# Kernel optimization log

Measured on AMD Instinct MI355X. Metric: run time of the kernel, lower is better.

Reference implementation:

```python
import jax, jax.numpy as jnp
import numpy as np

T, D, H, E, K = 4096, 1024, 2048, 8, 2  # tokens, model dim, expert hidden, n_experts, top_k
AUX_COEF = 0.01


def setup_inputs() -> dict:
    key = jax.random.key(0)
    ks = jax.random.split(key, 8)
    sd = lambda fan_in: 1.0 / np.sqrt(fan_in)
    x = jax.random.normal(ks[0], (T, D), jnp.float32)
    Wr = jax.random.normal(ks[1], (E, D), jnp.float32) * sd(D)      # router (no bias)
    w1 = jax.random.normal(ks[2], (E, H, D), jnp.float32) * sd(D)   # stacked up-proj
    w2 = jax.random.normal(ks[3], (E, D, H), jnp.float32) * sd(H)   # stacked down-proj
    w3 = jax.random.normal(ks[4], (E, H, D), jnp.float32) * sd(D)   # stacked gate-proj
    w1s = jax.random.normal(ks[5], (H, D), jnp.float32) * sd(D)     # shared expert
    w2s = jax.random.normal(ks[6], (D, H), jnp.float32) * sd(H)
    w3s = jax.random.normal(ks[7], (H, D), jnp.float32) * sd(D)
    return dict(x=x, Wr=Wr, w1=w1, w2=w2, w3=w3, w1s=w1s, w2s=w2s, w3s=w3s)


def _gelu(v):
    return jax.nn.gelu(v, approximate=False)  # torch F.gelu default = exact erf


def reference(x, Wr, w1, w2, w3, w1s, w2s, w3s):
    n_tok = x.shape[0]
    router_out = x @ Wr.T                                   # [T, E]
    router_probs = jax.nn.softmax(router_out, axis=-1)
    _, topk_idx = jax.lax.top_k(router_out, K)              # [T, K]
    topk_probs, _ = jax.lax.top_k(router_probs, K)          # top-k of probs (same order)

    # auxiliary load-balance loss (first-choice density * mean prob)
    expert_mask = jax.nn.one_hot(topk_idx[:, 0], E, dtype=jnp.float32)
    density = expert_mask.mean(axis=0)
    aux_loss = AUX_COEF * jnp.sum(density * router_probs.mean(axis=0)) * E

    # combine weights C[t, e] = sum of routed probs for expert e at token t
    C = jnp.zeros((n_tok, E), x.dtype).at[
        jnp.arange(n_tok)[:, None], topk_idx
    ].add(topk_probs)

    # dense per-expert SwiGLU-style FFN, combined by C (equal math to
    # sort-based dispatch + scatter_add in the original)
    h = _gelu(jnp.einsum('td,ehd->teh', x, w1)) * jnp.einsum('td,ehd->teh', x, w3)
    ye = jnp.einsum('teh,edh->ted', h, w2)                  # [T, E, D]
    out = jnp.einsum('ted,te->td', ye, C)

    # shared expert (always active)
    out = out + (_gelu(x @ w1s.T) * (x @ w3s.T)) @ w2s.T
    return out, aux_loss
```

## Files before the change

kernel.cpp:

```cpp
#include <hip/hip_runtime.h>
#include <hip/hip_bf16.h>
#include <cstdint>

#define T_TOK 4096
#define DMODEL 1024
#define HDIM 2048

typedef short bf16x8 __attribute__((ext_vector_type(8)));
typedef float f32x4 __attribute__((ext_vector_type(4)));
typedef uint32_t u32x4 __attribute__((ext_vector_type(4)));

__device__ __forceinline__ uint32_t cvt_pk_bf16(float lo, float hi) {
  uint32_t d;
  asm("v_cvt_pk_bf16_f32 %0, %1, %2" : "=v"(d) : "v"(lo), "v"(hi));
  return d;
}
__device__ __forceinline__ unsigned short f2bf(float f) {
  uint32_t d;
  asm("v_cvt_pk_bf16_f32 %0, %1, %1" : "=v"(d) : "v"(f));
  return (unsigned short)d;
}
__device__ __forceinline__ float gelu_fast(float v) {
  float z = v * 0.70710678118654752f;
  float az = fabsf(z);
  float t = __frcp_rn(1.0f + 0.3275911f * az);
  float poly = ((((1.061405429f * t - 1.453152027f) * t + 1.421413741f) * t
                 - 0.284496736f) * t + 0.254829592f) * t;
  float er = 1.0f - poly * __expf(-z * z);
  er = (z < 0.f) ? -er : er;
  return 0.5f * v * (1.0f + er);
}
__device__ __forceinline__ void gload16(const void* g, void* lds) {
  __builtin_amdgcn_global_load_lds((const __attribute__((address_space(1))) void*)g,
                                   (__attribute__((address_space(3))) void*)lds, 16, 0, 0);
}
__device__ __forceinline__ u32x4 pk8(const float* s) {
  float4 v0 = ((const float4*)s)[0], v1 = ((const float4*)s)[1];
  u32x4 p = {cvt_pk_bf16(v0.x, v0.y), cvt_pk_bf16(v0.z, v0.w),
             cvt_pk_bf16(v1.x, v1.y), cvt_pk_bf16(v1.z, v1.w)};
  return p;
}
__device__ __forceinline__ int xcd_remap(int d, int nblk) {
  int q = nblk >> 3, r = nblk & 7, xc = d & 7, i = d >> 3;
  return (xc < r ? xc * (q + 1) : r * (q + 1) + (xc - r) * q) + i;
}

__global__ __launch_bounds__(256) void convert_w(
    const float* __restrict__ w1, const float* __restrict__ w3,
    const float* __restrict__ w1s, const float* __restrict__ w3s,
    const float* __restrict__ w2, const float* __restrict__ w2s,
    short* __restrict__ wB, short* __restrict__ wd) {
  int bid = blockIdx.x;
  if (bid < 18432) {
    int id = bid * 256 + threadIdx.x;
    int e = id >> 19, rem = id & 524287;
    int nf = rem >> 11, k32 = (rem >> 6) & 31, ln = rem & 63;
    int h = (nf >> 1) * 16 + (ln & 15);
    size_t so = (size_t)h * DMODEL + k32 * 32 + (ln >> 4) * 8;
    const float* src = (nf & 1)
        ? ((e < 8) ? w3 + (size_t)e * 2097152 + so : w3s + so)
        : ((e < 8) ? w1 + (size_t)e * 2097152 + so : w1s + so);
    *(u32x4*)(wB + (size_t)id * 8) = pk8(src);
  } else {
    int id = (bid - 18432) * 256 + threadIdx.x;
    int e = id >> 18, rem = id & 262143;
    int d16 = rem >> 12, h32 = (rem >> 6) & 63, ln = rem & 63;
    size_t so = (size_t)(d16 * 16 + (ln & 15)) * HDIM + h32 * 32 + (ln >> 4) * 8;
    const float* s2 = (e < 8) ? w2 + (size_t)e * 2097152 + so : w2s + so;
    *(u32x4*)(wd + (size_t)id * 8) = pk8(s2);
  }
}

__global__ __launch_bounds__(256) void router_kernel(
    const float* __restrict__ x, const float* __restrict__ Wr,
    int* __restrict__ cursor, int* __restrict__ cnt1,
    float* __restrict__ psum, int* __restrict__ perm,
    int* __restrict__ tokpos, float* __restrict__ wtok,
    short* __restrict__ xb) {
  __shared__ float4 sW[8 * 256];
  __shared__ float sP[8];
  int tid = threadIdx.x;
  const float4* W4 = (const float4*)Wr;
  for (int i = tid; i < 2048; i += 256) sW[i] = W4[i];
  if (tid < 8) sP[tid] = 0.f;
  __syncthreads();

  int lane = tid & 63, wid = tid >> 6;
  int t = blockIdx.x * 4 + wid;
  float acc[8] = {0.f, 0.f, 0.f, 0.f, 0.f, 0.f, 0.f, 0.f};
  const float4* x4 = (const float4*)(x + (size_t)t * DMODEL);
#pragma unroll
  for (int it = 0; it < 4; ++it) {
    float4 xv = x4[it * 64 + lane];
    uint2 pk = {cvt_pk_bf16(xv.x, xv.y), cvt_pk_bf16(xv.z, xv.w)};
    *(uint2*)(xb + (size_t)t * DMODEL + it * 256 + lane * 4) = pk;
#pragma unroll
    for (int e = 0; e < 8; ++e) {
      float4 wv = sW[e * 256 + it * 64 + lane];
      acc[e] += xv.x * wv.x + xv.y * wv.y + xv.z * wv.z + xv.w * wv.w;
    }
  }
#pragma unroll
  for (int e = 0; e < 8; ++e)
    for (int off = 32; off; off >>= 1) acc[e] += __shfl_xor(acc[e], off);

  float mx = acc[0];
#pragma unroll
  for (int e = 1; e < 8; ++e) mx = fmaxf(mx, acc[e]);
  float ex[8], s = 0.f;
#pragma unroll
  for (int e = 0; e < 8; ++e) { ex[e] = expf(acc[e] - mx); s += ex[e]; }
  float inv = 1.f / s;
  int e0 = 0;
#pragma unroll
  for (int e = 1; e < 8; ++e) if (acc[e] > acc[e0]) e0 = e;
  int e1 = (e0 == 0) ? 1 : 0;
#pragma unroll
  for (int e = 0; e < 8; ++e) if (e != e0 && acc[e] > acc[e1]) e1 = e;

  if (lane == 0) {
#pragma unroll
    for (int e = 0; e < 8; ++e) atomicAdd(&sP[e], ex[e] * inv);
    atomicAdd(&cnt1[e0], 1);
    int s0 = atomicAdd(&cursor[e0], 1);
    perm[e0 * 4096 + s0] = t;
    int s1 = atomicAdd(&cursor[e1], 1);
    perm[e1 * 4096 + s1] = t;
    tokpos[2 * t] = (e0 << 12) | s0;
    tokpos[2 * t + 1] = (e1 << 12) | s1;
    wtok[2 * t] = ex[e0] * inv;
    wtok[2 * t + 1] = ex[e1] * inv;
  }
  __syncthreads();
  if (tid < 8) atomicAdd(&psum[tid], sP[tid]);
}

__global__ void finalize_kernel(const int* __restrict__ cursor,
                                const int* __restrict__ cnt1,
                                const float* __restrict__ psum,
                                int* __restrict__ base,
                                int* __restrict__ work, int* __restrict__ nwork,
                                float* __restrict__ aux_out) {
  if (threadIdx.x == 0) {
    int b = 0, a = 0;
    for (int e = 0; e < 9; ++e) {
      int c = (e < 8) ? cursor[e] : 4096;
      base[e] = b;
      int t1 = (c + 127) >> 7;
      for (int mt = 0; mt < t1; ++mt) work[a++] = (e << 8) | mt;
      b += t1 << 7;
    }
    *nwork = a;
    float aux = 0.f;
    for (int e = 0; e < 8; ++e)
      aux += ((float)cnt1[e] * (1.f / T_TOK)) * (psum[e] * (1.f / T_TOK));
    aux_out[0] = 0.01f * 8.f * aux;
  }
}

__global__ __launch_bounds__(256, 3) void gemm_upgate(
    const short* __restrict__ xb, const short* __restrict__ wB,
    const int* __restrict__ cursor, const int* __restrict__ base,
    const int* __restrict__ work, const int* __restrict__ nwork,
    const int* __restrict__ perm, unsigned short* __restrict__ hbuf) {
  int nblk = *nwork * 32;
  int d = blockIdx.x;
  if (d >= nblk) return;
  int o = xcd_remap(d, nblk);
  int y = o >> 5, nt = o & 31;
  int wk = work[y];
  int e = wk >> 8, mt = wk & 255;
  int cnt = (e < 8) ? cursor[e] : 4096;
  int hb = base[e];
  const short* wE = wB + (size_t)e * 4194304;

  __shared__ short lds[16384];

  int tid = threadIdx.x, lane = tid & 63, wid = tid >> 6;
  int fr = lane & 15, q4r = lane >> 4;
  int wm = wid >> 1, wn = wid & 1;

  size_t aOff[2], bOff[2];
#pragma unroll
  for (int c = 0; c < 2; ++c) {
    int g = c * 4 + wid;
    int slot = mt * 128 + g * 16 + fr;
    int tok = (e == 8) ? slot : ((slot < cnt) ? perm[e * 4096 + slot] : 0);
    aOff[c] = (size_t)tok * DMODEL + q4r * 8;
    bOff[c] = (size_t)(nt * 8 + g) * 32 * 512 + lane * 8;
  }

  auto stage = [&](int b, int t) {
#pragma unroll
    for (int c = 0; c < 2; ++c) {
      int g = c * 4 + wid;
      gload16(xb + aOff[c] + t * 32, &lds[b * 8192 + g * 512 + lane * 8]);
      gload16(wE + bOff[c] + (size_t)t * 512,
              &lds[b * 8192 + 4096 + g * 512 + lane * 8]);
    }
  };

  f32x4 acc[4][4] = {};

  auto compute = [&](int b) {
    bf16x8 af[4], bf[4];
#pragma unroll
    for (int m = 0; m < 4; ++m)
      af[m] = *(const bf16x8*)&lds[b * 8192 + (wm * 4 + m) * 512 + lane * 8];
#pragma unroll
    for (int n = 0; n < 4; ++n)
      bf[n] = *(const bf16x8*)&lds[b * 8192 + 4096 + (wn * 4 + n) * 512 + lane * 8];
    __builtin_amdgcn_s_setprio(1);
#pragma unroll
    for (int m = 0; m < 4; ++m)
#pragma unroll
      for (int n = 0; n < 4; ++n)
        acc[m][n] = __builtin_amdgcn_mfma_f32_16x16x32_bf16(af[m], bf[n], acc[m][n], 0, 0, 0);
    __builtin_amdgcn_s_setprio(0);
  };

  stage(0, 0);
  __syncthreads();
  int b = 0;
#pragma unroll 1
  for (int t = 0; t < 32; ++t) {
    if (t < 31) stage(b ^ 1, t + 1);
    compute(b);
    __syncthreads();
    b ^= 1;
  }

#pragma unroll
  for (int m = 0; m < 4; ++m) {
#pragma unroll
    for (int p = 0; p < 2; ++p) {
      f32x4 u = acc[m][2 * p], g = acc[m][2 * p + 1];
      int hcol = (nt * 4 + wn * 2 + p) * 16 + fr;
#pragma unroll
      for (int j = 0; j < 4; ++j) {
        int sl = mt * 128 + wm * 64 + m * 16 + q4r * 4 + j;
        float hv = (sl < cnt) ? gelu_fast(u[j]) * g[j] : 0.f;
        hbuf[(size_t)(hb + sl) * HDIM + hcol] = f2bf(hv);
      }
    }
  }
}

__global__ __launch_bounds__(256, 3) void gemm_down(
    const unsigned short* __restrict__ hbuf, const short* __restrict__ wd,
    const int* __restrict__ base,
    const int* __restrict__ work, const int* __restrict__ nwork,
    float* __restrict__ ybuf) {
  int nblk = *nwork * 8;
  int d = blockIdx.x;
  if (d >= nblk) return;
  int o = xcd_remap(d, nblk);
  int y = o >> 3, nt = o & 7;
  int wk = work[y];
  int e = wk >> 8, mt = wk & 255;
  int hb = base[e];
  const short* wdE = wd + (size_t)e * 2097152;

  __shared__ short lds[16384];

  int tid = threadIdx.x, lane = tid & 63, wid = tid >> 6;
  int fr = lane & 15, q4r = lane >> 4;
  int wm = wid >> 1, wn = wid & 1;

  size_t aOff[2], bOff[2];
#pragma unroll
  for (int c = 0; c < 2; ++c) {
    int g = c * 4 + wid;
    aOff[c] = (size_t)(hb + mt * 128 + g * 16 + fr) * HDIM + q4r * 8;
    bOff[c] = (size_t)(nt * 8 + g) * 64 * 512 + lane * 8;
  }

  auto stage = [&](int b, int t) {
#pragma unroll
    for (int c = 0; c < 2; ++c) {
      int g = c * 4 + wid;
      gload16(hbuf + aOff[c] + t * 32, &lds[b * 8192 + g * 512 + lane * 8]);
      gload16(wdE + bOff[c] + (size_t)t * 512,
              &lds[b * 8192 + 4096 + g * 512 + lane * 8]);
    }
  };

  f32x4 acc[4][4] = {};

  auto compute = [&](int b) {
    bf16x8 af[4], bf[4];
#pragma unroll
    for (int m = 0; m < 4; ++m)
      af[m] = *(const bf16x8*)&lds[b * 8192 + (wm * 4 + m) * 512 + lane * 8];
#pragma unroll
    for (int n = 0; n < 4; ++n)
      bf[n] = *(const bf16x8*)&lds[b * 8192 + 4096 + (wn * 4 + n) * 512 + lane * 8];
    __builtin_amdgcn_s_setprio(1);
#pragma unroll
    for (int m = 0; m < 4; ++m)
#pragma unroll
      for (int n = 0; n < 4; ++n)
        acc[m][n] = __builtin_amdgcn_mfma_f32_16x16x32_bf16(af[m], bf[n], acc[m][n], 0, 0, 0);
    __builtin_amdgcn_s_setprio(0);
  };

  stage(0, 0);
  __syncthreads();
  int b = 0;
#pragma unroll 1
  for (int t = 0; t < 64; ++t) {
    if (t < 63) stage(b ^ 1, t + 1);
    compute(b);
    __syncthreads();
    b ^= 1;
  }

#pragma unroll
  for (int m = 0; m < 4; ++m) {
#pragma unroll
    for (int n = 0; n < 4; ++n) {
      int col = (nt * 8 + wn * 4 + n) * 16 + fr;
      f32x4 a = acc[m][n];
#pragma unroll
      for (int j = 0; j < 4; ++j) {
        int row = mt * 128 + wm * 64 + m * 16 + q4r * 4 + j;
        ybuf[(size_t)(hb + row) * DMODEL + col] = a[j];
      }
    }
  }
}

__global__ __launch_bounds__(256) void gather_kernel(
    const float* __restrict__ ybuf, const int* __restrict__ tokpos,
    const float* __restrict__ wtok, const int* __restrict__ base,
    float* __restrict__ out) {
  int t = blockIdx.x, c4 = threadIdx.x;
  int p0 = tokpos[2 * t], p1 = tokpos[2 * t + 1];
  float w0 = wtok[2 * t], w1 = wtok[2 * t + 1];
  size_t r0 = (size_t)(base[p0 >> 12] + (p0 & 4095)) * DMODEL;
  size_t r1 = (size_t)(base[p1 >> 12] + (p1 & 4095)) * DMODEL;
  size_t rs = (size_t)(base[8] + t) * DMODEL;
  float4 v0 = *(const float4*)(ybuf + r0 + c4 * 4);
  float4 v1 = *(const float4*)(ybuf + r1 + c4 * 4);
  float4 vs = *(const float4*)(ybuf + rs + c4 * 4);
  float4 o;
  o.x = w0 * v0.x + w1 * v1.x + vs.x;
  o.y = w0 * v0.y + w1 * v1.y + vs.y;
  o.z = w0 * v0.z + w1 * v1.z + vs.z;
  o.w = w0 * v0.w + w1 * v1.w + vs.w;
  *(float4*)(out + (size_t)t * DMODEL + c4 * 4) = o;
}

extern "C" void kernel_launch(void* const* d_in, const int* in_sizes, int n_in,
                              void* d_out, int out_size, void* d_ws, size_t ws_size,
                              hipStream_t stream) {
  const float* x   = (const float*)d_in[0];
  const float* Wr  = (const float*)d_in[1];
  const float* w1  = (const float*)d_in[2];
  const float* w2  = (const float*)d_in[3];
  const float* w3  = (const float*)d_in[4];
  const float* w1s = (const float*)d_in[5];
  const float* w2s = (const float*)d_in[6];
  const float* w3s = (const float*)d_in[7];
  float* out = (float*)d_out;

  char* ws = (char*)d_ws;
  const size_t HBUF_OFF = 0;
  const size_t XB_OFF   = 58720256;
  const size_t WB_OFF   = XB_OFF + 8388608;
  const size_t WD_OFF   = WB_OFF + 75497472;
  const size_t PERM_OFF = WD_OFF + 37748736;
  const size_t TP_OFF   = PERM_OFF + 131072;
  const size_t WT_OFF   = TP_OFF + 32768;
  const size_t CTRL_OFF = WT_OFF + 32768;
  const size_t WORK_OFF = CTRL_OFF + 256;

  unsigned short* hbuf = (unsigned short*)(ws + HBUF_OFF);
  short* xb = (short*)(ws + XB_OFF);
  short* wB = (short*)(ws + WB_OFF);
  short* wd = (short*)(ws + WD_OFF);
  float* ybuf = (float*)(ws + WB_OFF);
  int*   perm   = (int*)(ws + PERM_OFF);
  int*   tokpos = (int*)(ws + TP_OFF);
  float* wtok   = (float*)(ws + WT_OFF);
  int*   cursor = (int*)(ws + CTRL_OFF);
  int*   cnt1   = (int*)(ws + CTRL_OFF + 64);
  float* psum   = (float*)(ws + CTRL_OFF + 128);
  int*   base   = (int*)(ws + CTRL_OFF + 192);
  int*   nwork  = (int*)(ws + CTRL_OFF + 240);
  int*   work   = (int*)(ws + WORK_OFF);

  hipMemsetAsync(ws + CTRL_OFF, 0, 256, stream);

  router_kernel<<<1024, 256, 0, stream>>>(x, Wr, cursor, cnt1, psum, perm,
                                          tokpos, wtok, xb);
  finalize_kernel<<<1, 64, 0, stream>>>(cursor, cnt1, psum, base, work, nwork,
                                        out + (size_t)T_TOK * DMODEL);
  convert_w<<<27648, 256, 0, stream>>>(w1, w3, w1s, w3s, w2, w2s, wB, wd);
  gemm_upgate<<<3328, 256, 0, stream>>>(xb, wB, cursor, base, work, nwork,
                                        perm, hbuf);
  gemm_down<<<832, 256, 0, stream>>>(hbuf, wd, base, work, nwork, ybuf);
  gather_kernel<<<4096, 256, 0, stream>>>(ybuf, tokpos, wtok, base, out);
}
```

Measured before the change: 405.8 us.

## Fuse router with weight conversion, use 256x256 down GEMM with bf16 output

Router and weight conversion now run in one kernel launch, so routing blocks overlap with the conversion work. Expert groups are padded to 256 rows and the down projection becomes a 512-thread, 256x256-tile kernel. It has a 128KB double-buffered LDS pipeline driven by explicit vmcnt waits and barriers, aimed at cutting B-matrix refetch and raising MFMA density. The intermediate y buffer is stored as bf16 instead of fp32 to halve gather traffic, and upgate launch bounds go to 4 waves per SIMD. The risks are lower output precision, more padded rows per expert, and low occupancy in the large-tile kernel.

```diff
diff --git a/kernel.cpp b/kernel.cpp
--- a/kernel.cpp
+++ b/kernel.cpp
@@ -9,6 +9,9 @@
 typedef short bf16x8 __attribute__((ext_vector_type(8)));
 typedef float f32x4 __attribute__((ext_vector_type(4)));
 typedef uint32_t u32x4 __attribute__((ext_vector_type(4)));
+
+#define WAITVM(N) asm volatile("s_waitcnt vmcnt(" #N ")" ::: "memory")
+#define BARX() asm volatile("s_barrier" ::: "memory")
 
 __device__ __forceinline__ uint32_t cvt_pk_bf16(float lo, float hi) {
   uint32_t d;
@@ -19,6 +22,9 @@
   uint32_t d;
   asm("v_cvt_pk_bf16_f32 %0, %1, %1" : "=v"(d) : "v"(f));
   return (unsigned short)d;
+}
+__device__ __forceinline__ float bf2f(unsigned short u) {
+  return __uint_as_float((uint32_t)u << 16);
 }
 __device__ __forceinline__ float gelu_fast(float v) {
   float z = v * 0.70710678118654752f;
@@ -45,48 +51,51 @@
   return (xc < r ? xc * (q + 1) : r * (q + 1) + (xc - r) * q) + i;
 }
 
-__global__ __launch_bounds__(256) void convert_w(
+__global__ __launch_bounds__(256) void prep_kernel(
+    const float* __restrict__ x, const float* __restrict__ Wr,
     const float* __restrict__ w1, const float* __restrict__ w3,
     const float* __restrict__ w1s, const float* __restrict__ w3s,
     const float* __restrict__ w2, const float* __restrict__ w2s,
-    short* __restrict__ wB, short* __restrict__ wd) {
-  int bid = blockIdx.x;
-  if (bid < 18432) {
-    int id = bid * 256 + threadIdx.x;
-    int e = id >> 19, rem = id & 524287;
-    int nf = rem >> 11, k32 = (rem >> 6) & 31, ln = rem & 63;
-    int h = (nf >> 1) * 16 + (ln & 15);
-    size_t so = (size_t)h * DMODEL + k32 * 32 + (ln >> 4) * 8;
-    const float* src = (nf & 1)
-        ? ((e < 8) ? w3 + (size_t)e * 2097152 + so : w3s + so)
-        : ((e < 8) ? w1 + (size_t)e * 2097152 + so : w1s + so);
-    *(u32x4*)(wB + (size_t)id * 8) = pk8(src);
-  } else {
-    int id = (bid - 18432) * 256 + threadIdx.x;
-    int e = id >> 18, rem = id & 262143;
-    int d16 = rem >> 12, h32 = (rem >> 6) & 63, ln = rem & 63;
-    size_t so = (size_t)(d16 * 16 + (ln & 15)) * HDIM + h32 * 32 + (ln >> 4) * 8;
-    const float* s2 = (e < 8) ? w2 + (size_t)e * 2097152 + so : w2s + so;
-    *(u32x4*)(wd + (size_t)id * 8) = pk8(s2);
-  }
-}
-
-__global__ __launch_bounds__(256) void router_kernel(
-    const float* __restrict__ x, const float* __restrict__ Wr,
+    short* __restrict__ wB, short* __restrict__ wd,
     int* __restrict__ cursor, int* __restrict__ cnt1,
     float* __restrict__ psum, int* __restrict__ perm,
     int* __restrict__ tokpos, float* __restrict__ wtok,
     short* __restrict__ xb) {
   __shared__ float4 sW[8 * 256];
   __shared__ float sP[8];
+  int bid = blockIdx.x;
   int tid = threadIdx.x;
+
+  if (bid >= 1024) {
+    int cbid = bid - 1024;
+    if (cbid < 18432) {
+      int id = cbid * 256 + tid;
+      int e = id >> 19, rem = id & 524287;
+      int nf = rem >> 11, k32 = (rem >> 6) & 31, ln = rem & 63;
+      int h = (nf >> 1) * 16 + (ln & 15);
+      size_t so = (size_t)h * DMODEL + k32 * 32 + (ln >> 4) * 8;
+      const float* src = (nf & 1)
+          ? ((e < 8) ? w3 + (size_t)e * 2097152 + so : w3s + so)
+          : ((e < 8) ? w1 + (size_t)e * 2097152 + so : w1s + so);
+      *(u32x4*)(wB + (size_t)id * 8) = pk8(src);
+    } else {
+      int id = (cbid - 18432) * 256 + tid;
+      int e = id >> 18, rem = id & 262143;
+      int d16 = rem >> 12, h32 = (rem >> 6) & 63, ln = rem & 63;
+      size_t so = (size_t)(d16 * 16 + (ln & 15)) * HDIM + h32 * 32 + (ln >> 4) * 8;
+      const float* s2 = (e < 8) ? w2 + (size_t)e * 2097152 + so : w2s + so;
+      *(u32x4*)(wd + (size_t)id * 8) = pk8(s2);
+    }
+    return;
+  }
+
   const float4* W4 = (const float4*)Wr;
   for (int i = tid; i < 2048; i += 256) sW[i] = W4[i];
   if (tid < 8) sP[tid] = 0.f;
   __syncthreads();
 
   int lane = tid & 63, wid = tid >> 6;
-  int t = blockIdx.x * 4 + wid;
+  int t = bid * 4 + wid;
   float acc[8] = {0.f, 0.f, 0.f, 0.f, 0.f, 0.f, 0.f, 0.f};
   const float4* x4 = (const float4*)(x + (size_t)t * DMODEL);
 #pragma unroll
@@ -139,18 +148,21 @@
                                 const int* __restrict__ cnt1,
                                 const float* __restrict__ psum,
                                 int* __restrict__ base,
-                                int* __restrict__ work, int* __restrict__ nwork,
+                                int* __restrict__ work128, int* __restrict__ n128,
+                                int* __restrict__ work256, int* __restrict__ n256,
                                 float* __restrict__ aux_out) {
   if (threadIdx.x == 0) {
-    int b = 0, a = 0;
+    int b = 0, a1 = 0, a2 = 0;
     for (int e = 0; e < 9; ++e) {
       int c = (e < 8) ? cursor[e] : 4096;
       base[e] = b;
       int t1 = (c + 127) >> 7;
-      for (int mt = 0; mt < t1; ++mt) work[a++] = (e << 8) | mt;
-      b += t1 << 7;
-    }
-    *nwork = a;
+      for (int mt = 0; mt < t1; ++mt) work128[a1++] = (e << 8) | mt;
+      int t2 = (c + 255) >> 8;
+      for (int mt = 0; mt < t2; ++mt) work256[a2++] = (e << 8) | mt;
+      b += t2 << 8;
+    }
+    *n128 = a1; *n256 = a2;
     float aux = 0.f;
     for (int e = 0; e < 8; ++e)
       aux += ((float)cnt1[e] * (1.f / T_TOK)) * (psum[e] * (1.f / T_TOK));
@@ -158,7 +170,7 @@
   }
 }
 
-__global__ __launch_bounds__(256, 3) void gemm_upgate(
+__global__ __launch_bounds__(256, 4) void gemm_upgate(
     const short* __restrict__ xb, const short* __restrict__ wB,
     const int* __restrict__ cursor, const int* __restrict__ base,
     const int* __restrict__ work, const int* __restrict__ nwork,
@@ -246,92 +258,104 @@
   }
 }
 
-__global__ __launch_bounds__(256, 3) void gemm_down(
+__global__ __launch_bounds__(512) void gemm_down8(
     const unsigned short* __restrict__ hbuf, const short* __restrict__ wd,
     const int* __restrict__ base,
     const int* __restrict__ work, const int* __restrict__ nwork,
-    float* __restrict__ ybuf) {
-  int nblk = *nwork * 8;
-  int d = blockIdx.x;
-  if (d >= nblk) return;
-  int o = xcd_remap(d, nblk);
-  int y = o >> 3, nt = o & 7;
+    unsigned short* __restrict__ yb) {
+  int y = blockIdx.y;
+  if (y >= *nwork) return;
   int wk = work[y];
-  int e = wk >> 8, mt = wk & 255;
+  int e = wk >> 8, mt = wk & 255, nt = blockIdx.x;
   int hb = base[e];
   const short* wdE = wd + (size_t)e * 2097152;
 
-  __shared__ short lds[16384];
+  __shared__ short lds[65536];
 
   int tid = threadIdx.x, lane = tid & 63, wid = tid >> 6;
+  int wm = wid >> 2, wn = wid & 3;
   int fr = lane & 15, q4r = lane >> 4;
-  int wm = wid >> 1, wn = wid & 1;
-
-  size_t aOff[2], bOff[2];
-#pragma unroll
-  for (int c = 0; c < 2; ++c) {
-    int g = c * 4 + wid;
-    aOff[c] = (size_t)(hb + mt * 128 + g * 16 + fr) * HDIM + q4r * 8;
-    bOff[c] = (size_t)(nt * 8 + g) * 64 * 512 + lane * 8;
-  }
-
-  auto stage = [&](int b, int t) {
-#pragma unroll
-    for (int c = 0; c < 2; ++c) {
-      int g = c * 4 + wid;
-      gload16(hbuf + aOff[c] + t * 32, &lds[b * 8192 + g * 512 + lane * 8]);
-      gload16(wdE + bOff[c] + (size_t)t * 512,
-              &lds[b * 8192 + 4096 + g * 512 + lane * 8]);
-    }
-  };
-
-  f32x4 acc[4][4] = {};
-
-  auto compute = [&](int b) {
-    bf16x8 af[4], bf[4];
-#pragma unroll
-    for (int m = 0; m < 4; ++m)
-      af[m] = *(const bf16x8*)&lds[b * 8192 + (wm * 4 + m) * 512 + lane * 8];
-#pragma unroll
-    for (int n = 0; n < 4; ++n)
-      bf[n] = *(const bf16x8*)&lds[b * 8192 + 4096 + (wn * 4 + n) * 512 + lane * 8];
-    __builtin_amdgcn_s_setprio(1);
-#pragma unroll
-    for (int m = 0; m < 4; ++m)
-#pragma unroll
-      for (int n = 0; n < 4; ++n)
-        acc[m][n] = __builtin_amdgcn_mfma_f32_16x16x32_bf16(af[m], bf[n], acc[m][n], 0, 0, 0);
-    __builtin_amdgcn_s_setprio(0);
-  };
-
-  stage(0, 0);
-  __syncthreads();
-  int b = 0;
+
+  size_t aOff[2];
+#pragma unroll
+  for (int c = 0; c < 2; ++c)
+    aOff[c] = (size_t)(hb + mt * 256 + (c * 8 + wid) * 16 + fr) * HDIM + q4r * 8;
+  size_t bOff[2];
+#pragma unroll
+  for (int c = 0; c < 2; ++c)
+    bOff[c] = ((size_t)(nt * 16 + c * 8 + wid) * 64) * 512 + lane * 8;
+
+#define DWN_STAGE_A(tt, k32)                                                   \
+  { int bb_ = ((tt) & 1) * 32768;                                              \
+    gload16(hbuf + aOff[0] + (tt) * 64 + (k32) * 32,                           \
+            &lds[bb_ + ((k32) * 16 + wid) * 512 + lane * 8]);                  \
+    gload16(hbuf + aOff[1] + (tt) * 64 + (k32) * 32,                           \
+            &lds[bb_ + ((k32) * 16 + 8 + wid) * 512 + lane * 8]); }
+#define DWN_STAGE_B(tt, k32)                                                   \
+  { int bb_ = ((tt) & 1) * 32768;                                              \
+    gload16(wdE + bOff[0] + (size_t)((tt) * 2 + (k32)) * 512,                  \
+            &lds[bb_ + 16384 + ((k32) * 16 + wid) * 512 + lane * 8]);          \
+    gload16(wdE + bOff[1] + (size_t)((tt) * 2 + (k32)) * 512,                  \
+            &lds[bb_ + 16384 + ((k32) * 16 + 8 + wid) * 512 + lane * 8]); }
+#define DWN_READA(k32, mh)                                                     \
+  { _Pragma("unroll") for (int i = 0; i < 4; ++i)                              \
+      af[i] = *(const bf16x8*)&lds[bb + ((k32) * 16 + wm * 8 + (mh) * 4 + i) * \
+                                       512 + lane * 8]; }
+#define DWN_READB(k32)                                                         \
+  { _Pragma("unroll") for (int n = 0; n < 4; ++n)                              \
+      bf[n] = *(const bf16x8*)&lds[bb + 16384 + ((k32) * 16 + wn * 4 + n) *    \
+                                       512 + lane * 8]; }
+#define DWN_MFMA(mh)                                                           \
+  { __builtin_amdgcn_s_setprio(1);                                             \
+    _Pragma("unroll") for (int i = 0; i < 4; ++i)                              \
+      _Pragma("unroll") for (int n = 0; n < 4; ++n)                            \
+        acc[(mh) * 4 + i][n] = __builtin_amdgcn_mfma_f32_16x16x32_bf16(        \
+            af[i], bf[n], acc[(mh) * 4 + i][n], 0, 0, 0);                      \
+    __builtin_amdgcn_s_setprio(0); }
+
+  f32x4 acc[8][4] = {};
+  bf16x8 af[4], bf[4];
+
+  DWN_STAGE_A(0, 0); DWN_STAGE_B(0, 0); DWN_STAGE_A(0, 1); DWN_STAGE_B(0, 1);
+  WAITVM(4); BARX();
+
 #pragma unroll 1
-  for (int t = 0; t < 64; ++t) {
-    if (t < 63) stage(b ^ 1, t + 1);
-    compute(b);
-    __syncthreads();
-    b ^= 1;
-  }
-
-#pragma unroll
-  for (int m = 0; m < 4; ++m) {
+  for (int t = 0; t < 31; ++t) {
+    const int bb = (t & 1) * 32768;
+    DWN_READA(0, 0); DWN_READB(0); DWN_STAGE_A(t + 1, 0);
+    BARX(); DWN_MFMA(0); BARX();
+    DWN_READA(0, 1); DWN_STAGE_B(t + 1, 0);
+    BARX(); DWN_MFMA(1); WAITVM(4); BARX();
+    DWN_READA(1, 0); DWN_READB(1); DWN_STAGE_A(t + 1, 1);
+    BARX(); DWN_MFMA(0); BARX();
+    DWN_READA(1, 1); DWN_STAGE_B(t + 1, 1);
+    BARX(); DWN_MFMA(1); WAITVM(4); BARX();
+  }
+  {
+    const int bb = 32768;
+    DWN_READA(0, 0); DWN_READB(0); BARX(); DWN_MFMA(0); BARX();
+    DWN_READA(0, 1); BARX(); DWN_MFMA(1); WAITVM(0); BARX();
+    DWN_READA(1, 0); DWN_READB(1); BARX(); DWN_MFMA(0); BARX();
+    DWN_READA(1, 1); DWN_MFMA(1);
+  }
+
+#pragma unroll
+  for (int m = 0; m < 8; ++m) {
 #pragma unroll
     for (int n = 0; n < 4; ++n) {
-      int col = (nt * 8 + wn * 4 + n) * 16 + fr;
+      int col = (nt * 16 + wn * 4 + n) * 16 + fr;
       f32x4 a = acc[m][n];
 #pragma unroll
       for (int j = 0; j < 4; ++j) {
-        int row = mt * 128 + wm * 64 + m * 16 + q4r * 4 + j;
-        ybuf[(size_t)(hb + row) * DMODEL + col] = a[j];
+        int row = mt * 256 + wm * 128 + m * 16 + q4r * 4 + j;
+        yb[(size_t)(hb + row) * DMODEL + col] = f2bf(a[j]);
       }
     }
   }
 }
 
 __global__ __launch_bounds__(256) void gather_kernel(
-    const float* __restrict__ ybuf, const int* __restrict__ tokpos,
+    const unsigned short* __restrict__ yb, const int* __restrict__ tokpos,
     const float* __restrict__ wtok, const int* __restrict__ base,
     float* __restrict__ out) {
   int t = blockIdx.x, c4 = threadIdx.x;
@@ -340,14 +364,14 @@
   size_t r0 = (size_t)(base[p0 >> 12] + (p0 & 4095)) * DMODEL;
   size_t r1 = (size_t)(base[p1 >> 12] + (p1 & 4095)) * DMODEL;
   size_t rs = (size_t)(base[8] + t) * DMODEL;
-  float4 v0 = *(const float4*)(ybuf + r0 + c4 * 4);
-  float4 v1 = *(const float4*)(ybuf + r1 + c4 * 4);
-  float4 vs = *(const float4*)(ybuf + rs + c4 * 4);
+  ushort4 v0 = *(const ushort4*)(yb + r0 + c4 * 4);
+  ushort4 v1 = *(const ushort4*)(yb + r1 + c4 * 4);
+  ushort4 vs = *(const ushort4*)(yb + rs + c4 * 4);
   float4 o;
-  o.x = w0 * v0.x + w1 * v1.x + vs.x;
-  o.y = w0 * v0.y + w1 * v1.y + vs.y;
-  o.z = w0 * v0.z + w1 * v1.z + vs.z;
-  o.w = w0 * v0.w + w1 * v1.w + vs.w;
+  o.x = w0 * bf2f(v0.x) + w1 * bf2f(v1.x) + bf2f(vs.x);
+  o.y = w0 * bf2f(v0.y) + w1 * bf2f(v1.y) + bf2f(vs.y);
+  o.z = w0 * bf2f(v0.z) + w1 * bf2f(v1.z) + bf2f(vs.z);
+  o.w = w0 * bf2f(v0.w) + w1 * bf2f(v1.w) + bf2f(vs.w);
   *(float4*)(out + (size_t)t * DMODEL + c4 * 4) = o;
 }
 
@@ -373,13 +397,14 @@
   const size_t TP_OFF   = PERM_OFF + 131072;
   const size_t WT_OFF   = TP_OFF + 32768;
   const size_t CTRL_OFF = WT_OFF + 32768;
-  const size_t WORK_OFF = CTRL_OFF + 256;
+  const size_t W128_OFF = CTRL_OFF + 256;
+  const size_t W256_OFF = W128_OFF + 512;
 
   unsigned short* hbuf = (unsigned short*)(ws + HBUF_OFF);
   short* xb = (short*)(ws + XB_OFF);
   short* wB = (short*)(ws + WB_OFF);
   short* wd = (short*)(ws + WD_OFF);
-  float* ybuf = (float*)(ws + WB_OFF);
+  unsigned short* yb = (unsigned short*)(ws + WB_OFF);
   int*   perm   = (int*)(ws + PERM_OFF);
   int*   tokpos = (int*)(ws + TP_OFF);
   float* wtok   = (float*)(ws + WT_OFF);
@@ -387,18 +412,21 @@
   int*   cnt1   = (int*)(ws + CTRL_OFF + 64);
   float* psum   = (float*)(ws + CTRL_OFF + 128);
   int*   base   = (int*)(ws + CTRL_OFF + 192);
-  int*   nwork  = (int*)(ws + CTRL_OFF + 240);
-  int*   work   = (int*)(ws + WORK_OFF);
+  int*   n128   = (int*)(ws + CTRL_OFF + 236);
+  int*   n256   = (int*)(ws + CTRL_OFF + 240);
+  int*   work128 = (int*)(ws + W128_OFF);
+  int*   work256 = (int*)(ws + W256_OFF);
 
   hipMemsetAsync(ws + CTRL_OFF, 0, 256, stream);
 
-  router_kernel<<<1024, 256, 0, stream>>>(x, Wr, cursor, cnt1, psum, perm,
-                                          tokpos, wtok, xb);
-  finalize_kernel<<<1, 64, 0, stream>>>(cursor, cnt1, psum, base, work, nwork,
+  prep_kernel<<<28672, 256, 0, stream>>>(x, Wr, w1, w3, w1s, w3s, w2, w2s,
+                                         wB, wd, cursor, cnt1, psum, perm,
+                                         tokpos, wtok, xb);
+  finalize_kernel<<<1, 64, 0, stream>>>(cursor, cnt1, psum, base,
+                                        work128, n128, work256, n256,
                                         out + (size_t)T_TOK * DMODEL);
-  convert_w<<<27648, 256, 0, stream>>>(w1, w3, w1s, w3s, w2, w2s, wB, wd);
-  gemm_upgate<<<3328, 256, 0, stream>>>(xb, wB, cursor, base, work, nwork,
+  gemm_upgate<<<3328, 256, 0, stream>>>(xb, wB, cursor, base, work128, n128,
                                         perm, hbuf);
-  gemm_down<<<832, 256, 0, stream>>>(hbuf, wd, base, work, nwork, ybuf);
-  gather_kernel<<<4096, 256, 0, stream>>>(ybuf, tokpos, wtok, base, out);
-}
+  gemm_down8<<<dim3(4, 64), 512, 0, stream>>>(hbuf, wd, base, work256, n256, yb);
+  gather_kernel<<<4096, 256, 0, stream>>>(yb, tokpos, wtok, base, out);
+}
```

Measured after the change: 381.4 us. 6.0% less time.
